# Kernel tuning notes

Measured on AMD Instinct MI355X. Metric: run time of the kernel, lower is better.

## Reference

```python
import jax, jax.numpy as jnp
import numpy as np

N_NODES = 50000
N_EDGES = 1600000
DIM_NODE = 64
DIM_HIDDEN = [64, 64]
EDGE_DIM = 32
NUM_CLASSES = 10
NUM_GRAPHS = 128


def _glorot(key, shape):
    fan_in, fan_out = shape[0], shape[1]
    lim = jnp.sqrt(6.0 / (fan_in + fan_out))
    return jax.random.uniform(key, shape, jnp.float32, -lim, lim)


def setup_inputs() -> dict:
    key = jax.random.key(0)
    ks = jax.random.split(key, 20)
    x = jax.random.normal(ks[0], (N_NODES, DIM_NODE), jnp.float32)
    edge_attr = jax.random.normal(ks[1], (N_EDGES, EDGE_DIM), jnp.float32)
    edge_index = jax.random.randint(ks[2], (2, N_EDGES), 0, N_NODES, jnp.int64)
    batch = jnp.sort(jax.random.randint(ks[3], (N_NODES,), 0, NUM_GRAPHS, jnp.int64))
    h0 = (DIM_NODE + DIM_HIDDEN[0]) // 2  # 64
    h1 = (DIM_HIDDEN[0] + DIM_HIDDEN[1]) // 2  # 64
    return {
        "x": x,
        "edge_attr": edge_attr,
        "We1": _glorot(ks[4], (EDGE_DIM, DIM_NODE)), "be1": jnp.zeros((DIM_NODE,), jnp.float32),
        "W1a": _glorot(ks[5], (DIM_NODE, h0)), "b1a": jnp.zeros((h0,), jnp.float32),
        "W1b": _glorot(ks[6], (h0, DIM_HIDDEN[0])), "b1b": jnp.zeros((DIM_HIDDEN[0],), jnp.float32),
        "We2": _glorot(ks[7], (EDGE_DIM, DIM_HIDDEN[0])), "be2": jnp.zeros((DIM_HIDDEN[0],), jnp.float32),
        "W2a": _glorot(ks[8], (DIM_HIDDEN[0], h1)), "b2a": jnp.zeros((h1,), jnp.float32),
        "W2b": _glorot(ks[9], (h1, DIM_HIDDEN[1])), "b2b": jnp.zeros((DIM_HIDDEN[1],), jnp.float32),
        "Wf": _glorot(ks[10], (DIM_HIDDEN[1], NUM_CLASSES)), "bf": jnp.zeros((NUM_CLASSES,), jnp.float32),
        "edge_index": edge_index,
        "batch": batch,
    }


def _gine_conv(x, edge_index, edge_attr, We, be, Wa, ba, Wb, bb):
    # PyG GINEConv (eps=0): msg = relu(x_src + lin_edge(edge_attr)),
    # aggr = scatter_sum(msg -> dst), out = nn(x + aggr)
    src, dst = edge_index[0], edge_index[1]
    e = edge_attr @ We + be                      # [E, d]
    m = jax.nn.relu(x[src] + e)                  # [E, d] gather + add + relu
    aggr = jax.ops.segment_sum(m, dst, num_segments=x.shape[0])  # [N, d]
    h = x + aggr
    h = h @ Wa + ba
    h = h @ Wb + bb
    return h


def reference(x, edge_attr, We1, be1, W1a, b1a, W1b, b1b,
              We2, be2, W2a, b2a, W2b, b2b, Wf, bf,
              edge_index, batch):
    h = jax.nn.relu(_gine_conv(x, edge_index, edge_attr, We1, be1, W1a, b1a, W1b, b1b))
    h = jax.nn.relu(_gine_conv(h, edge_index, edge_attr, We2, be2, W2a, b2a, W2b, b2b))
    # global mean pool per graph
    sums = jax.ops.segment_sum(h, batch, num_segments=NUM_GRAPHS)
    cnts = jax.ops.segment_sum(jnp.ones((h.shape[0],), h.dtype), batch, num_segments=NUM_GRAPHS)
    pooled = sums / jnp.clip(cnts, 1.0)[:, None]
    # ffn: (dropout p=0 in eval) -> linear -> softmax
    logits = pooled @ Wf + bf
    return jax.nn.softmax(logits, axis=1)
```

## Files before the change

kernel.cpp:

```cpp
#include <hip/hip_runtime.h>

#define N_NODES 50000
#define N_EDGES 1600000
#define DIM 64
#define EDIM 32
#define NUM_GRAPHS 128
#define NUM_CLASSES 10
#define NBIN_PAD 50176
#define NSCAN_BLK 196
#define EPAD_MAX 2200000
#define NBUCK 196
#define BCAP 12288
#define ACH 4096

typedef __attribute__((ext_vector_type(8))) short bf16x8;
typedef __attribute__((ext_vector_type(4))) short short4v;
typedef __attribute__((ext_vector_type(4))) unsigned short ushort4v;
typedef __attribute__((ext_vector_type(4))) float f32x4;

static __device__ __forceinline__ short f2bf(float f) {
    unsigned u = __builtin_bit_cast(unsigned, f);
    u += 0x7fff + ((u >> 16) & 1);
    return (short)(u >> 16);
}
static __device__ __forceinline__ float bf2f(short s) {
    unsigned u = ((unsigned)(unsigned short)s) << 16;
    return __builtin_bit_cast(float, u);
}
static __device__ __forceinline__ int cvt_pk_bf16(float lo, float hi) {
    int r;
    asm("v_cvt_pk_bf16_f32 %0, %1, %2" : "=v"(r) : "v"(lo), "v"(hi));
    return r;
}

__global__ void __launch_bounds__(256) binA_kernel(
    const int* __restrict__ src, const int* __restrict__ dst,
    int* __restrict__ bcur, int2* __restrict__ bbuf)
{
    __shared__ int hist[256];
    __shared__ int scanb[256];
    __shared__ int bexcl[256];
    __shared__ int cursA[256];
    __shared__ int gbase[256];
    __shared__ int2 st[ACH];

    const int t = threadIdx.x;
    const int e0 = blockIdx.x * ACH;
    const int nv = min(ACH, N_EDGES - e0);

    hist[t] = 0;
    __syncthreads();

    int w1[ACH / 256];
    #pragma unroll
    for (int i = 0; i < ACH / 256; ++i) {
        int idx = t + 256 * i;
        if (idx < nv) {
            int e = e0 + idx;
            int d = dst[e], s = src[e];
            w1[i] = (s & 0xFFFF) | (d << 16);
            atomicAdd(&hist[(unsigned)w1[i] >> 24], 1);
        } else {
            w1[i] = -1;
        }
    }
    __syncthreads();

    int v = hist[t];
    scanb[t] = v;
    __syncthreads();
    #pragma unroll
    for (int off = 1; off < 256; off <<= 1) {
        int add = (t >= off) ? scanb[t - off] : 0;
        __syncthreads();
        scanb[t] += add;
        __syncthreads();
    }
    int excl = scanb[t] - v;
    bexcl[t] = excl;
    cursA[t] = excl;
    if (v > 0) gbase[t] = atomicAdd(&bcur[t], v);
    __syncthreads();

    #pragma unroll
    for (int i = 0; i < ACH / 256; ++i) {
        int idx = t + 256 * i;
        if (idx < nv) {
            int b = (unsigned)w1[i] >> 24;
            int r = atomicAdd(&cursA[b], 1);
            int2 rec; rec.x = e0 + idx; rec.y = w1[i];
            st[r] = rec;
        }
    }
    __syncthreads();

    for (int k = t; k < nv; k += 256) {
        int2 rec = st[k];
        int b = (unsigned)rec.y >> 24;
        int pos = gbase[b] + (k - bexcl[b]);
        if (pos < BCAP) bbuf[(size_t)b * BCAP + pos] = rec;
    }
}

__global__ void __launch_bounds__(1024) binB1_kernel(
    const int* __restrict__ bcur, const int2* __restrict__ bbuf,
    int* __restrict__ cnt)
{
    __shared__ int nodecnt[256];
    const int b = blockIdx.x, t = threadIdx.x;
    if (t < 256) nodecnt[t] = 0;
    __syncthreads();
    const int nb = min(bcur[b], BCAP);
    for (int k = t; k < nb; k += 1024) {
        int2 rec = bbuf[(size_t)b * BCAP + k];
        int dlow = ((unsigned)rec.y >> 16) & 0xFF;
        atomicAdd(&nodecnt[dlow], 1);
    }
    __syncthreads();
    if (t < 256) cnt[b * 256 + t] = nodecnt[t];
}

__global__ void scan_part(const int* __restrict__ cnt, int* __restrict__ pstart,
                          int* __restrict__ partial) {
    __shared__ int sh[256];
    const int b = blockIdx.x, t = threadIdx.x;
    const int i = b * 256 + t;
    int v = ((cnt[i] + 15) >> 4) << 4;
    sh[t] = v;
    __syncthreads();
    #pragma unroll
    for (int off = 1; off < 256; off <<= 1) {
        int add = (t >= off) ? sh[t - off] : 0;
        __syncthreads();
        sh[t] += add;
        __syncthreads();
    }
    pstart[i] = sh[t] - v;
    if (t == 255) partial[b] = sh[t];
}

__global__ void scan_mid(int* __restrict__ partial) {
    __shared__ int sh[256];
    const int t = threadIdx.x;
    int v = (t < NSCAN_BLK) ? partial[t] : 0;
    sh[t] = v;
    __syncthreads();
    #pragma unroll
    for (int off = 1; off < 256; off <<= 1) {
        int add = (t >= off) ? sh[t - off] : 0;
        __syncthreads();
        sh[t] += add;
        __syncthreads();
    }
    if (t < NSCAN_BLK) partial[t] = sh[t] - v;
}

__global__ void scan_add(int* __restrict__ pstart, const int* __restrict__ partial) {
    const int b = blockIdx.x, t = threadIdx.x;
    const int i = b * 256 + t;
    pstart[i] += partial[b];
}

__global__ void __launch_bounds__(1024) binB2_kernel(
    const int* __restrict__ bcur, const int2* __restrict__ bbuf,
    const int* __restrict__ pstart, const int* __restrict__ cnt,
    const float* __restrict__ ea,
    unsigned short* __restrict__ ssrc, short* __restrict__ eab,
    int* __restrict__ tnode, float* __restrict__ aggr)
{
    __shared__ int cur[256];
    const int b = blockIdx.x, t = threadIdx.x;
    if (t < 256) cur[t] = pstart[b * 256 + t];
    __syncthreads();
    const int nb = min(bcur[b], BCAP);
    for (int k = t; k < nb; k += 1024) {
        int2 rec = bbuf[(size_t)b * BCAP + k];
        unsigned y = (unsigned)rec.y;
        int dlow = (y >> 16) & 0xFF;
        int p = atomicAdd(&cur[dlow], 1);
        ssrc[p] = (unsigned short)(y & 0xFFFF);
        const float* ar = ea + (size_t)rec.x * EDIM;
        int* er = (int*)(eab + (size_t)p * 32);
        #pragma unroll
        for (int qq = 0; qq < 4; ++qq) {
            float4 lo = *reinterpret_cast<const float4*>(ar + 4 * qq);
            float4 hi = *reinterpret_cast<const float4*>(ar + 4 * qq + 16);
            int4 w;
            w.x = cvt_pk_bf16(lo.x, lo.y);
            w.y = cvt_pk_bf16(lo.z, lo.w);
            w.z = cvt_pk_bf16(hi.x, hi.y);
            w.w = cvt_pk_bf16(hi.z, hi.w);
            *reinterpret_cast<int4*>(er + 4 * qq) = w;
        }
    }
    __syncthreads();
    if (t < 256) {
        int n = b * 256 + t;
        if (n < N_NODES) {
            int p0 = pstart[n], deg = cnt[n];
            int pe = p0 + (((deg + 15) >> 4) << 4);
            int4 z; z.x = 0; z.y = 0; z.z = 0; z.w = 0;
            for (int p = p0 + deg; p < pe; ++p) {
                ssrc[p] = (unsigned short)N_NODES;
                int4* er = (int4*)(eab + (size_t)p * 32);
                er[0] = z; er[1] = z; er[2] = z; er[3] = z;
            }
            for (int tt = p0 >> 4; tt < (pe >> 4); ++tt) tnode[tt] = n;
            if (deg == 0) {
                float4 z4; z4.x = 0.f; z4.y = 0.f; z4.z = 0.f; z4.w = 0.f;
                float4* arow = (float4*)(aggr + (size_t)n * 64);
                #pragma unroll
                for (int j = 0; j < 16; ++j) arow[j] = z4;
            }
        }
    }
}

__global__ void xprep_kernel(const float* __restrict__ x, short* __restrict__ xb,
                             short* __restrict__ hb) {
    int t = blockIdx.x * blockDim.x + threadIdx.x;
    if (t >= (N_NODES + 1) * 64) return;
    int n = t >> 6, k = t & 63;
    if (n == N_NODES) {
        short pz = f2bf(-1e30f);
        xb[t] = pz;
        hb[t] = pz;
        return;
    }
    int dim = 16 * (k & 3) + (k >> 2);
    xb[(size_t)n * 64 + k] = f2bf(x[(size_t)n * 64 + dim]);
}

__global__ void __launch_bounds__(256) edge_kernel(
    const short* __restrict__ xb,
    const short* __restrict__ eab,
    const unsigned short* __restrict__ ssrc,
    const float* __restrict__ We,
    const float* __restrict__ be,
    const int*   __restrict__ tnode,
    const int*   __restrict__ pstart,
    float* __restrict__ aggr)
{
    const int lane = threadIdx.x & 63;
    const int q = lane >> 4;
    const int c = lane & 15;
    const int wave  = (blockIdx.x * blockDim.x + threadIdx.x) >> 6;
    const int nwav  = (gridDim.x * blockDim.x) >> 6;

    const int ntiles = pstart[N_NODES] >> 4;
    int t0 = (int)(((long long)ntiles * wave) / nwav);
    int t1 = (int)(((long long)ntiles * (wave + 1)) / nwav);
    while (t0 > 0 && t0 < ntiles && tnode[t0] == tnode[t0 - 1]) ++t0;
    while (t1 > 0 && t1 < ntiles && tnode[t1] == tnode[t1 - 1]) ++t1;
    if (t0 >= t1) return;

    bf16x8 bfrag[4];
    #pragma unroll
    for (int t = 0; t < 4; ++t) {
        #pragma unroll
        for (int e = 0; e < 8; ++e) {
            int k = 4 * q + (e & 3) + 16 * (e >> 2);
            bfrag[t][e] = f2bf(We[k * 64 + 16 * t + c]);
        }
    }
    f32x4 cb[4];
    #pragma unroll
    for (int t = 0; t < 4; ++t) {
        float bv = be[16 * t + c];
        cb[t][0] = bv; cb[t][1] = bv; cb[t][2] = bv; cb[t][3] = bv;
    }

    auto clampT = [&](int tt) { return tt < t1 ? tt : t1 - 1; };
    auto loadIdx = [&](int tt, int& tn, ushort4v& s4) {
        tn = tnode[tt];
        s4 = *reinterpret_cast<const ushort4v*>(ssrc + tt * 16 + 4 * q);
    };
    auto loadE = [&](int tt) {
        return *reinterpret_cast<const bf16x8*>(eab + (size_t)tt * 512 + c * 32 + q * 8);
    };

    int prev_n = -1;
    float acc0 = 0.f, acc1 = 0.f, acc2 = 0.f, acc3 = 0.f;

    auto flush = [&](int n) {
        float r0 = acc0 + __shfl_xor(acc0, 16, 64);
        float r1 = acc1 + __shfl_xor(acc1, 16, 64);
        float r2 = acc2 + __shfl_xor(acc2, 16, 64);
        float r3 = acc3 + __shfl_xor(acc3, 16, 64);
        r0 += __shfl_xor(r0, 32, 64);
        r1 += __shfl_xor(r1, 32, 64);
        r2 += __shfl_xor(r2, 32, 64);
        r3 += __shfl_xor(r3, 32, 64);
        float v = (q == 0) ? r0 : (q == 1) ? r1 : (q == 2) ? r2 : r3;
        aggr[(size_t)n * 64 + lane] = v;
    };

    int tnA, tnB;
    ushort4v s4A, s4B;
    loadIdx(t0, tnA, s4A);
    loadIdx(clampT(t0 + 1), tnB, s4B);
    bf16x8 efA = loadE(t0);
    short4v xvA0 = *reinterpret_cast<const short4v*>(xb + (size_t)s4A.x * 64 + 4 * c);
    short4v xvA1 = *reinterpret_cast<const short4v*>(xb + (size_t)s4A.y * 64 + 4 * c);
    short4v xvA2 = *reinterpret_cast<const short4v*>(xb + (size_t)s4A.z * 64 + 4 * c);
    short4v xvA3 = *reinterpret_cast<const short4v*>(xb + (size_t)s4A.w * 64 + 4 * c);

    for (int tile = t0; tile < t1; ++tile) {
        bf16x8 efB = loadE(clampT(tile + 1));
        short4v yv0 = *reinterpret_cast<const short4v*>(xb + (size_t)s4B.x * 64 + 4 * c);
        short4v yv1 = *reinterpret_cast<const short4v*>(xb + (size_t)s4B.y * 64 + 4 * c);
        short4v yv2 = *reinterpret_cast<const short4v*>(xb + (size_t)s4B.z * 64 + 4 * c);
        short4v yv3 = *reinterpret_cast<const short4v*>(xb + (size_t)s4B.w * 64 + 4 * c);
        int tnC; ushort4v s4C;
        loadIdx(clampT(tile + 2), tnC, s4C);

        if (tnA != prev_n) {
            if (prev_n >= 0) flush(prev_n);
            prev_n = tnA;
            acc0 = acc1 = acc2 = acc3 = 0.f;
        }

        f32x4 d[4];
        #pragma unroll
        for (int t = 0; t < 4; ++t)
            d[t] = __builtin_amdgcn_mfma_f32_16x16x32_bf16(efA, bfrag[t], cb[t], 0, 0, 0);

        const short4v xv[4] = {xvA0, xvA1, xvA2, xvA3};
        #pragma unroll
        for (int r = 0; r < 4; ++r) {
            acc0 += fmaxf(d[0][r] + bf2f(xv[r][0]), 0.f);
            acc1 += fmaxf(d[1][r] + bf2f(xv[r][1]), 0.f);
            acc2 += fmaxf(d[2][r] + bf2f(xv[r][2]), 0.f);
            acc3 += fmaxf(d[3][r] + bf2f(xv[r][3]), 0.f);
        }

        tnA = tnB; s4A = s4B;
        tnB = tnC; s4B = s4C;
        efA = efB;
        xvA0 = yv0; xvA1 = yv1; xvA2 = yv2; xvA3 = yv3;
    }
    if (prev_n >= 0) flush(prev_n);
}

__global__ void __launch_bounds__(256) node_kernel(
    const float* __restrict__ x,
    const float* __restrict__ aggr,
    const float* __restrict__ Wab,
    const float* __restrict__ bab,
    float* __restrict__ out,
    short* __restrict__ hb)
{
    const int lane = threadIdx.x & 63;
    const int q = lane >> 4;
    const int c = lane & 15;
    const int wave = (blockIdx.x * blockDim.x + threadIdx.x) >> 6;
    const int nwav = (gridDim.x * blockDim.x) >> 6;

    bf16x8 bfrag[2][4];
    #pragma unroll
    for (int kk = 0; kk < 2; ++kk) {
        #pragma unroll
        for (int t = 0; t < 4; ++t) {
            #pragma unroll
            for (int e = 0; e < 8; ++e) {
                int k = 32 * kk + 4 * q + (e & 3) + 16 * (e >> 2);
                bfrag[kk][t][e] = f2bf(Wab[k * 64 + 16 * t + c]);
            }
        }
    }
    f32x4 cb[4];
    #pragma unroll
    for (int t = 0; t < 4; ++t) {
        float bv = bab[16 * t + c];
        cb[t][0] = bv; cb[t][1] = bv; cb[t][2] = bv; cb[t][3] = bv;
    }

    const int ntile = N_NODES / 16;
    for (int nt = wave; nt < ntile; nt += nwav) {
        const int n0 = nt * 16;
        const float* xr = x    + (size_t)(n0 + c) * 64;
        const float* ar = aggr + (size_t)(n0 + c) * 64;
        float4 v[4];
        #pragma unroll
        for (int j = 0; j < 4; ++j) {
            int off = (j >> 1) * 32 + (j & 1) * 16 + 4 * q;
            float4 a = *reinterpret_cast<const float4*>(xr + off);
            float4 b = *reinterpret_cast<const float4*>(ar + off);
            v[j].x = a.x + b.x; v[j].y = a.y + b.y;
            v[j].z = a.z + b.z; v[j].w = a.w + b.w;
        }
        f32x4 d[4];
        #pragma unroll
        for (int kk = 0; kk < 2; ++kk) {
            int4 ai;
            ai.x = cvt_pk_bf16(v[2 * kk].x, v[2 * kk].y);
            ai.y = cvt_pk_bf16(v[2 * kk].z, v[2 * kk].w);
            ai.z = cvt_pk_bf16(v[2 * kk + 1].x, v[2 * kk + 1].y);
            ai.w = cvt_pk_bf16(v[2 * kk + 1].z, v[2 * kk + 1].w);
            bf16x8 afrag = __builtin_bit_cast(bf16x8, ai);
            #pragma unroll
            for (int t = 0; t < 4; ++t)
                d[t] = __builtin_amdgcn_mfma_f32_16x16x32_bf16(
                    afrag, bfrag[kk][t], kk == 0 ? cb[t] : d[t], 0, 0, 0);
        }
        #pragma unroll
        for (int r = 0; r < 4; ++r) {
            float h0 = fmaxf(d[0][r], 0.f);
            float h1v = fmaxf(d[1][r], 0.f);
            float h2v = fmaxf(d[2][r], 0.f);
            float h3 = fmaxf(d[3][r], 0.f);
            float* orow = out + (size_t)(n0 + 4 * q + r) * 64;
            orow[c]      = h0;
            orow[16 + c] = h1v;
            orow[32 + c] = h2v;
            orow[48 + c] = h3;
            int2 pk;
            pk.x = cvt_pk_bf16(h0, h1v);
            pk.y = cvt_pk_bf16(h2v, h3);
            *reinterpret_cast<int2*>(hb + (size_t)(n0 + 4 * q + r) * 64 + 4 * c) = pk;
        }
    }
}

__global__ void prep_kernel(
    const float* __restrict__ Wa1, const float* __restrict__ ba1,
    const float* __restrict__ Wb1, const float* __restrict__ bb1,
    const float* __restrict__ Wa2, const float* __restrict__ ba2,
    const float* __restrict__ Wb2, const float* __restrict__ bb2,
    float* __restrict__ Wab1, float* __restrict__ bab1,
    float* __restrict__ Wab2, float* __restrict__ bab2)
{
    const int t = threadIdx.x;
    for (int idx = t; idx < 64 * 64; idx += 256) {
        int i = idx >> 6, j = idx & 63;
        float s1 = 0.f, s2 = 0.f;
        for (int m = 0; m < 64; ++m) {
            s1 += Wa1[i * 64 + m] * Wb1[m * 64 + j];
            s2 += Wa2[i * 64 + m] * Wb2[m * 64 + j];
        }
        Wab1[idx] = s1; Wab2[idx] = s2;
    }
    for (int j = t; j < 64; j += 256) {
        float s1 = bb1[j], s2 = bb2[j];
        for (int m = 0; m < 64; ++m) {
            s1 += ba1[m] * Wb1[m * 64 + j];
            s2 += ba2[m] * Wb2[m * 64 + j];
        }
        bab1[j] = s1; bab2[j] = s2;
    }
}

__global__ void __launch_bounds__(256) pool_kernel(
    const float* __restrict__ h,
    const int*   __restrict__ batch,
    float* __restrict__ psum,
    float* __restrict__ pcnt)
{
    const int lane = threadIdx.x & 63;
    const int wave = (blockIdx.x * blockDim.x + threadIdx.x) >> 6;
    const int n0 = wave * 64;
    if (n0 >= N_NODES) return;
    const int nend = min(n0 + 64, N_NODES);

    int cur = batch[n0];
    float acc = 0.f;
    int cnt = 0;
    for (int n = n0; n < nend; ++n) {
        int b = batch[n];
        if (b != cur) {
            atomicAdd(&psum[(size_t)cur * 64 + lane], acc);
            if (lane == 0) atomicAdd(&pcnt[cur], (float)cnt);
            cur = b; acc = 0.f; cnt = 0;
        }
        acc += h[(size_t)n * 64 + lane];
        cnt++;
    }
    atomicAdd(&psum[(size_t)cur * 64 + lane], acc);
    if (lane == 0) atomicAdd(&pcnt[cur], (float)cnt);
}

__global__ void final_kernel(
    const float* __restrict__ psum, const float* __restrict__ pcnt,
    const float* __restrict__ Wf, const float* __restrict__ bfv,
    float* __restrict__ out)
{
    __shared__ float pooled[NUM_GRAPHS * 64];
    __shared__ float logits[NUM_GRAPHS * NUM_CLASSES];
    const int t = threadIdx.x;
    for (int idx = t; idx < NUM_GRAPHS * 64; idx += 256) {
        int g = idx >> 6;
        float cc = pcnt[g];
        cc = cc < 1.f ? 1.f : cc;
        pooled[idx] = psum[idx] / cc;
    }
    __syncthreads();
    for (int idx = t; idx < NUM_GRAPHS * NUM_CLASSES; idx += 256) {
        int g = idx / NUM_CLASSES, cc = idx % NUM_CLASSES;
        float acc = bfv[cc];
        for (int k = 0; k < 64; ++k)
            acc += pooled[g * 64 + k] * Wf[k * NUM_CLASSES + cc];
        logits[idx] = acc;
    }
    __syncthreads();
    if (t < NUM_GRAPHS) {
        float mx = -1e30f;
        for (int cc = 0; cc < NUM_CLASSES; ++cc)
            mx = fmaxf(mx, logits[t * NUM_CLASSES + cc]);
        float s = 0.f;
        float ex[NUM_CLASSES];
        for (int cc = 0; cc < NUM_CLASSES; ++cc) {
            ex[cc] = expf(logits[t * NUM_CLASSES + cc] - mx);
            s += ex[cc];
        }
        for (int cc = 0; cc < NUM_CLASSES; ++cc)
            out[t * NUM_CLASSES + cc] = ex[cc] / s;
    }
}

extern "C" void kernel_launch(void* const* d_in, const int* in_sizes, int n_in,
                              void* d_out, int out_size, void* d_ws, size_t ws_size,
                              hipStream_t stream) {
    const float* x   = (const float*)d_in[0];
    const float* ea  = (const float*)d_in[1];
    const float* We1 = (const float*)d_in[2];
    const float* be1 = (const float*)d_in[3];
    const float* W1a = (const float*)d_in[4];
    const float* b1a = (const float*)d_in[5];
    const float* W1b = (const float*)d_in[6];
    const float* b1b = (const float*)d_in[7];
    const float* We2 = (const float*)d_in[8];
    const float* be2 = (const float*)d_in[9];
    const float* W2a = (const float*)d_in[10];
    const float* b2a = (const float*)d_in[11];
    const float* W2b = (const float*)d_in[12];
    const float* b2b = (const float*)d_in[13];
    const float* Wf  = (const float*)d_in[14];
    const float* bfv = (const float*)d_in[15];
    const int* ei    = (const int*)d_in[16];
    const int* batch = (const int*)d_in[17];
    const int* src = ei;
    const int* dst = ei + N_EDGES;

    int* wsb = (int*)d_ws;
    float* aggr = (float*)wsb;
    float* h1   = (float*)(wsb + 3200000);
    float* h2   = (float*)(wsb + 6400000);
    short* eab  = (short*)(wsb + 9600000);
    int2*  bbuf = (int2*)(wsb + 44800000);
    short* xb   = (short*)(wsb + 49616896);
    short* hb1  = (short*)(wsb + 51216928);
    short* hb2  = (short*)(wsb + 52816960);
    unsigned short* ssrc = (unsigned short*)(wsb + 54416992);
    int* tnode  = wsb + 55516992;
    float* Wab1 = (float*)(wsb + 55654492);
    float* bab1 = Wab1 + 4096;
    float* Wab2 = bab1 + 64;
    float* bab2 = Wab2 + 4096;
    float* psum = bab2 + 64;
    float* pcnt = psum + 8192;
    int* cnt    = (int*)(pcnt + 128);
    int* pstart = cnt + NBIN_PAD;
    int* partial= pstart + NBIN_PAD;
    int* bcur   = partial + 256;

    float* out = (float*)d_out;

    hipMemsetAsync(bcur, 0, 256 * sizeof(int), stream);
    binA_kernel<<<(N_EDGES + ACH - 1) / ACH, 256, 0, stream>>>(src, dst, bcur, bbuf);
    binB1_kernel<<<NBUCK, 1024, 0, stream>>>(bcur, bbuf, cnt);
    scan_part<<<NSCAN_BLK, 256, 0, stream>>>(cnt, pstart, partial);
    scan_mid<<<1, 256, 0, stream>>>(partial);
    scan_add<<<NSCAN_BLK, 256, 0, stream>>>(pstart, partial);
    binB2_kernel<<<NBUCK, 1024, 0, stream>>>(bcur, bbuf, pstart, cnt, ea,
                                             ssrc, eab, tnode, aggr);
    xprep_kernel<<<((N_NODES + 1) * 64 + 255) / 256, 256, 0, stream>>>(x, xb, hb1);

    hipMemsetAsync(psum, 0, (8192 + 128) * sizeof(float), stream);
    prep_kernel<<<1, 256, 0, stream>>>(W1a, b1a, W1b, b1b, W2a, b2a, W2b, b2b,
                                       Wab1, bab1, Wab2, bab2);

    edge_kernel<<<2048, 256, 0, stream>>>(xb, eab, ssrc, We1, be1, tnode, pstart, aggr);
    node_kernel<<<512, 256, 0, stream>>>(x, aggr, Wab1, bab1, h1, hb1);

    edge_kernel<<<2048, 256, 0, stream>>>(hb1, eab, ssrc, We2, be2, tnode, pstart, aggr);
    node_kernel<<<512, 256, 0, stream>>>(h1, aggr, Wab2, bab2, h2, hb2);

    pool_kernel<<<196, 256, 0, stream>>>(h2, batch, psum, pcnt);
    final_kernel<<<1, 256, 0, stream>>>(psum, pcnt, Wf, bfv, out);
}
```

Measured before the change: 396.6 us.

## Precompute per-edge ranks and split edge placement into many parallel blocks

binB1 now records each edge's rank within its destination node, so the placement pass no longer needs shared-memory atomics. That lets placement run across 8x more blocks (196*8 blocks of 256 threads), each handling a slice of a bucket, with two edges per thread to overlap the gathers of edge attributes. Padding and tnode setup move to a separate kernel. The cost is an extra rank array written and read, plus one more launch. The rank16 buffer is placed after bcur in the workspace, and it is not visible whether that region is large enough.

```diff
diff --git a/kernel.cpp b/kernel.cpp
--- a/kernel.cpp
+++ b/kernel.cpp
@@ -12,6 +12,7 @@
 #define NBUCK 196
 #define BCAP 12288
 #define ACH 4096
+#define NSL 8
 
 typedef __attribute__((ext_vector_type(8))) short bf16x8;
 typedef __attribute__((ext_vector_type(4))) short short4v;
@@ -104,7 +105,7 @@
 
 __global__ void __launch_bounds__(1024) binB1_kernel(
     const int* __restrict__ bcur, const int2* __restrict__ bbuf,
-    int* __restrict__ cnt)
+    int* __restrict__ cnt, unsigned short* __restrict__ rank16)
 {
     __shared__ int nodecnt[256];
     const int b = blockIdx.x, t = threadIdx.x;
@@ -112,9 +113,11 @@
     __syncthreads();
     const int nb = min(bcur[b], BCAP);
     for (int k = t; k < nb; k += 1024) {
-        int2 rec = bbuf[(size_t)b * BCAP + k];
+        size_t i = (size_t)b * BCAP + k;
+        int2 rec = bbuf[i];
         int dlow = ((unsigned)rec.y >> 16) & 0xFF;
-        atomicAdd(&nodecnt[dlow], 1);
+        int r = atomicAdd(&nodecnt[dlow], 1);
+        rank16[i] = (unsigned short)r;
     }
     __syncthreads();
     if (t < 256) cnt[b * 256 + t] = nodecnt[t];
@@ -161,58 +164,90 @@
     pstart[i] += partial[b];
 }
 
-__global__ void __launch_bounds__(1024) binB2_kernel(
+__global__ void __launch_bounds__(256) place_kernel(
     const int* __restrict__ bcur, const int2* __restrict__ bbuf,
+    const unsigned short* __restrict__ rank16,
+    const int* __restrict__ pstart, const float* __restrict__ ea,
+    unsigned short* __restrict__ ssrc, short* __restrict__ eab)
+{
+    const int b  = blockIdx.x >> 3;
+    const int sl = blockIdx.x & (NSL - 1);
+    const int t  = threadIdx.x;
+    const int nb = min(bcur[b], BCAP);
+    const int chunk = (nb + NSL - 1) / NSL;
+    const int k0 = sl * chunk;
+    const int k1 = min(k0 + chunk, nb);
+
+    for (int k = k0 + t; k < k1; k += 512) {
+        const int kb = k + 256;
+        const bool has2 = kb < k1;
+        const size_t i1 = (size_t)b * BCAP + k;
+        const size_t i2 = has2 ? (size_t)b * BCAP + kb : i1;
+        int2 rec1 = bbuf[i1];
+        int2 rec2 = bbuf[i2];
+        int rk1 = rank16[i1];
+        int rk2 = rank16[i2];
+        unsigned y1 = (unsigned)rec1.y, y2 = (unsigned)rec2.y;
+        int n1 = (b << 8) | ((y1 >> 16) & 0xFF);
+        int n2 = (b << 8) | ((y2 >> 16) & 0xFF);
+        int p1 = pstart[n1] + rk1;
+        int p2 = pstart[n2] + rk2;
+        const float* ar1 = ea + (size_t)rec1.x * EDIM;
+        const float* ar2 = ea + (size_t)rec2.x * EDIM;
+        float4 v1[8], v2[8];
+        #pragma unroll
+        for (int qq = 0; qq < 4; ++qq) {
+            v1[qq]     = *reinterpret_cast<const float4*>(ar1 + 4 * qq);
+            v1[qq + 4] = *reinterpret_cast<const float4*>(ar1 + 4 * qq + 16);
+            v2[qq]     = *reinterpret_cast<const float4*>(ar2 + 4 * qq);
+            v2[qq + 4] = *reinterpret_cast<const float4*>(ar2 + 4 * qq + 16);
+        }
+        ssrc[p1] = (unsigned short)(y1 & 0xFFFF);
+        ssrc[p2] = (unsigned short)(y2 & 0xFFFF);
+        int* er1 = (int*)(eab + (size_t)p1 * 32);
+        int* er2 = (int*)(eab + (size_t)p2 * 32);
+        #pragma unroll
+        for (int qq = 0; qq < 4; ++qq) {
+            int4 w;
+            w.x = cvt_pk_bf16(v1[qq].x, v1[qq].y);
+            w.y = cvt_pk_bf16(v1[qq].z, v1[qq].w);
+            w.z = cvt_pk_bf16(v1[qq + 4].x, v1[qq + 4].y);
+            w.w = cvt_pk_bf16(v1[qq + 4].z, v1[qq + 4].w);
+            *reinterpret_cast<int4*>(er1 + 4 * qq) = w;
+        }
+        #pragma unroll
+        for (int qq = 0; qq < 4; ++qq) {
+            int4 w;
+            w.x = cvt_pk_bf16(v2[qq].x, v2[qq].y);
+            w.y = cvt_pk_bf16(v2[qq].z, v2[qq].w);
+            w.z = cvt_pk_bf16(v2[qq + 4].x, v2[qq + 4].y);
+            w.w = cvt_pk_bf16(v2[qq + 4].z, v2[qq + 4].w);
+            *reinterpret_cast<int4*>(er2 + 4 * qq) = w;
+        }
+    }
+}
+
+__global__ void __launch_bounds__(256) pad_kernel(
     const int* __restrict__ pstart, const int* __restrict__ cnt,
-    const float* __restrict__ ea,
     unsigned short* __restrict__ ssrc, short* __restrict__ eab,
     int* __restrict__ tnode, float* __restrict__ aggr)
 {
-    __shared__ int cur[256];
-    const int b = blockIdx.x, t = threadIdx.x;
-    if (t < 256) cur[t] = pstart[b * 256 + t];
-    __syncthreads();
-    const int nb = min(bcur[b], BCAP);
-    for (int k = t; k < nb; k += 1024) {
-        int2 rec = bbuf[(size_t)b * BCAP + k];
-        unsigned y = (unsigned)rec.y;
-        int dlow = (y >> 16) & 0xFF;
-        int p = atomicAdd(&cur[dlow], 1);
-        ssrc[p] = (unsigned short)(y & 0xFFFF);
-        const float* ar = ea + (size_t)rec.x * EDIM;
-        int* er = (int*)(eab + (size_t)p * 32);
-        #pragma unroll
-        for (int qq = 0; qq < 4; ++qq) {
-            float4 lo = *reinterpret_cast<const float4*>(ar + 4 * qq);
-            float4 hi = *reinterpret_cast<const float4*>(ar + 4 * qq + 16);
-            int4 w;
-            w.x = cvt_pk_bf16(lo.x, lo.y);
-            w.y = cvt_pk_bf16(lo.z, lo.w);
-            w.z = cvt_pk_bf16(hi.x, hi.y);
-            w.w = cvt_pk_bf16(hi.z, hi.w);
-            *reinterpret_cast<int4*>(er + 4 * qq) = w;
-        }
-    }
-    __syncthreads();
-    if (t < 256) {
-        int n = b * 256 + t;
-        if (n < N_NODES) {
-            int p0 = pstart[n], deg = cnt[n];
-            int pe = p0 + (((deg + 15) >> 4) << 4);
-            int4 z; z.x = 0; z.y = 0; z.z = 0; z.w = 0;
-            for (int p = p0 + deg; p < pe; ++p) {
-                ssrc[p] = (unsigned short)N_NODES;
-                int4* er = (int4*)(eab + (size_t)p * 32);
-                er[0] = z; er[1] = z; er[2] = z; er[3] = z;
-            }
-            for (int tt = p0 >> 4; tt < (pe >> 4); ++tt) tnode[tt] = n;
-            if (deg == 0) {
-                float4 z4; z4.x = 0.f; z4.y = 0.f; z4.z = 0.f; z4.w = 0.f;
-                float4* arow = (float4*)(aggr + (size_t)n * 64);
-                #pragma unroll
-                for (int j = 0; j < 16; ++j) arow[j] = z4;
-            }
-        }
+    int n = blockIdx.x * 256 + threadIdx.x;
+    if (n >= N_NODES) return;
+    int p0 = pstart[n], deg = cnt[n];
+    int pe = p0 + (((deg + 15) >> 4) << 4);
+    int4 z; z.x = 0; z.y = 0; z.z = 0; z.w = 0;
+    for (int p = p0 + deg; p < pe; ++p) {
+        ssrc[p] = (unsigned short)N_NODES;
+        int4* er = (int4*)(eab + (size_t)p * 32);
+        er[0] = z; er[1] = z; er[2] = z; er[3] = z;
+    }
+    for (int tt = p0 >> 4; tt < (pe >> 4); ++tt) tnode[tt] = n;
+    if (deg == 0) {
+        float4 z4; z4.x = 0.f; z4.y = 0.f; z4.z = 0.f; z4.w = 0.f;
+        float4* arow = (float4*)(aggr + (size_t)n * 64);
+        #pragma unroll
+        for (int j = 0; j < 16; ++j) arow[j] = z4;
     }
 }
 
@@ -562,17 +597,19 @@
     int* pstart = cnt + NBIN_PAD;
     int* partial= pstart + NBIN_PAD;
     int* bcur   = partial + 256;
+    unsigned short* rank16 = (unsigned short*)(bcur + 256);
 
     float* out = (float*)d_out;
 
     hipMemsetAsync(bcur, 0, 256 * sizeof(int), stream);
     binA_kernel<<<(N_EDGES + ACH - 1) / ACH, 256, 0, stream>>>(src, dst, bcur, bbuf);
-    binB1_kernel<<<NBUCK, 1024, 0, stream>>>(bcur, bbuf, cnt);
+    binB1_kernel<<<NBUCK, 1024, 0, stream>>>(bcur, bbuf, cnt, rank16);
     scan_part<<<NSCAN_BLK, 256, 0, stream>>>(cnt, pstart, partial);
     scan_mid<<<1, 256, 0, stream>>>(partial);
     scan_add<<<NSCAN_BLK, 256, 0, stream>>>(pstart, partial);
-    binB2_kernel<<<NBUCK, 1024, 0, stream>>>(bcur, bbuf, pstart, cnt, ea,
-                                             ssrc, eab, tnode, aggr);
+    place_kernel<<<NBUCK * NSL, 256, 0, stream>>>(bcur, bbuf, rank16, pstart, ea,
+                                                  ssrc, eab);
+    pad_kernel<<<NSCAN_BLK, 256, 0, stream>>>(pstart, cnt, ssrc, eab, tnode, aggr);
     xprep_kernel<<<((N_NODES + 1) * 64 + 255) / 256, 256, 0, stream>>>(x, xb, hb1);
 
     hipMemsetAsync(psum, 0, (8192 + 128) * sizeof(float), stream);
```

Result: no change. 403.4 us (+1.7%).

## Split edge binning into rank, position, coalesced edge-attr scatter, and pad kernels

Applied to the files above, without the earlier changes.

binB1 now records each edge's intra-node rank, so final positions can be computed without a second atomic pass. A new pos_kernel writes per-edge destination positions and source ids. A separate grid-wide kernel then reads edge_attr in original order (coalesced) and scatters bf16 rows, replacing random gathers done by only 196 blocks. Padding work moves to its own kernel; this adds extra launches and a pos buffer in the workspace.

```diff
diff --git a/kernel.cpp b/kernel.cpp
--- a/kernel.cpp
+++ b/kernel.cpp
@@ -104,7 +104,7 @@
 
 __global__ void __launch_bounds__(1024) binB1_kernel(
     const int* __restrict__ bcur, const int2* __restrict__ bbuf,
-    int* __restrict__ cnt)
+    int* __restrict__ cnt, unsigned short* __restrict__ rank16)
 {
     __shared__ int nodecnt[256];
     const int b = blockIdx.x, t = threadIdx.x;
@@ -112,9 +112,11 @@
     __syncthreads();
     const int nb = min(bcur[b], BCAP);
     for (int k = t; k < nb; k += 1024) {
-        int2 rec = bbuf[(size_t)b * BCAP + k];
+        size_t i = (size_t)b * BCAP + k;
+        int2 rec = bbuf[i];
         int dlow = ((unsigned)rec.y >> 16) & 0xFF;
-        atomicAdd(&nodecnt[dlow], 1);
+        int r = atomicAdd(&nodecnt[dlow], 1);
+        rank16[i] = (unsigned short)r;
     }
     __syncthreads();
     if (t < 256) cnt[b * 256 + t] = nodecnt[t];
@@ -161,58 +163,68 @@
     pstart[i] += partial[b];
 }
 
-__global__ void __launch_bounds__(1024) binB2_kernel(
+__global__ void __launch_bounds__(1024) pos_kernel(
     const int* __restrict__ bcur, const int2* __restrict__ bbuf,
+    const unsigned short* __restrict__ rank16, const int* __restrict__ pstart,
+    int* __restrict__ pos, unsigned short* __restrict__ ssrc)
+{
+    const int b = blockIdx.x, t = threadIdx.x;
+    const int nb = min(bcur[b], BCAP);
+    for (int k = t; k < nb; k += 1024) {
+        size_t i = (size_t)b * BCAP + k;
+        int2 rec = bbuf[i];
+        unsigned y = (unsigned)rec.y;
+        int n = (b << 8) | ((y >> 16) & 0xFF);
+        int p = pstart[n] + (int)rank16[i];
+        pos[rec.x] = p;
+        ssrc[p] = (unsigned short)(y & 0xFFFF);
+    }
+}
+
+__global__ void __launch_bounds__(256) eascatter_kernel(
+    const float* __restrict__ ea, const int* __restrict__ pos,
+    short* __restrict__ eab)
+{
+    int e = blockIdx.x * 256 + threadIdx.x;
+    if (e >= N_EDGES) return;
+    int p = pos[e];
+    if ((unsigned)p >= (unsigned)EPAD_MAX) return;
+    const float* ar = ea + (size_t)e * EDIM;
+    int4 w[4];
+    #pragma unroll
+    for (int qq = 0; qq < 4; ++qq) {
+        float4 lo = *reinterpret_cast<const float4*>(ar + 4 * qq);
+        float4 hi = *reinterpret_cast<const float4*>(ar + 4 * qq + 16);
+        w[qq].x = cvt_pk_bf16(lo.x, lo.y);
+        w[qq].y = cvt_pk_bf16(lo.z, lo.w);
+        w[qq].z = cvt_pk_bf16(hi.x, hi.y);
+        w[qq].w = cvt_pk_bf16(hi.z, hi.w);
+    }
+    int4* er = (int4*)(eab + (size_t)p * 32);
+    er[0] = w[0]; er[1] = w[1]; er[2] = w[2]; er[3] = w[3];
+}
+
+__global__ void __launch_bounds__(256) pad_kernel(
     const int* __restrict__ pstart, const int* __restrict__ cnt,
-    const float* __restrict__ ea,
     unsigned short* __restrict__ ssrc, short* __restrict__ eab,
     int* __restrict__ tnode, float* __restrict__ aggr)
 {
-    __shared__ int cur[256];
-    const int b = blockIdx.x, t = threadIdx.x;
-    if (t < 256) cur[t] = pstart[b * 256 + t];
-    __syncthreads();
-    const int nb = min(bcur[b], BCAP);
-    for (int k = t; k < nb; k += 1024) {
-        int2 rec = bbuf[(size_t)b * BCAP + k];
-        unsigned y = (unsigned)rec.y;
-        int dlow = (y >> 16) & 0xFF;
-        int p = atomicAdd(&cur[dlow], 1);
-        ssrc[p] = (unsigned short)(y & 0xFFFF);
-        const float* ar = ea + (size_t)rec.x * EDIM;
-        int* er = (int*)(eab + (size_t)p * 32);
-        #pragma unroll
-        for (int qq = 0; qq < 4; ++qq) {
-            float4 lo = *reinterpret_cast<const float4*>(ar + 4 * qq);
-            float4 hi = *reinterpret_cast<const float4*>(ar + 4 * qq + 16);
-            int4 w;
-            w.x = cvt_pk_bf16(lo.x, lo.y);
-            w.y = cvt_pk_bf16(lo.z, lo.w);
-            w.z = cvt_pk_bf16(hi.x, hi.y);
-            w.w = cvt_pk_bf16(hi.z, hi.w);
-            *reinterpret_cast<int4*>(er + 4 * qq) = w;
-        }
-    }
-    __syncthreads();
-    if (t < 256) {
-        int n = b * 256 + t;
-        if (n < N_NODES) {
-            int p0 = pstart[n], deg = cnt[n];
-            int pe = p0 + (((deg + 15) >> 4) << 4);
-            int4 z; z.x = 0; z.y = 0; z.z = 0; z.w = 0;
-            for (int p = p0 + deg; p < pe; ++p) {
-                ssrc[p] = (unsigned short)N_NODES;
-                int4* er = (int4*)(eab + (size_t)p * 32);
-                er[0] = z; er[1] = z; er[2] = z; er[3] = z;
-            }
-            for (int tt = p0 >> 4; tt < (pe >> 4); ++tt) tnode[tt] = n;
-            if (deg == 0) {
-                float4 z4; z4.x = 0.f; z4.y = 0.f; z4.z = 0.f; z4.w = 0.f;
-                float4* arow = (float4*)(aggr + (size_t)n * 64);
-                #pragma unroll
-                for (int j = 0; j < 16; ++j) arow[j] = z4;
-            }
-        }
+    int n = blockIdx.x * 256 + threadIdx.x;
+    if (n >= N_NODES) return;
+    int p0 = pstart[n], deg = cnt[n];
+    int pe = p0 + (((deg + 15) >> 4) << 4);
+    int4 z; z.x = 0; z.y = 0; z.z = 0; z.w = 0;
+    for (int p = p0 + deg; p < pe; ++p) {
+        ssrc[p] = (unsigned short)N_NODES;
+        int4* er = (int4*)(eab + (size_t)p * 32);
+        er[0] = z; er[1] = z; er[2] = z; er[3] = z;
+    }
+    for (int tt = p0 >> 4; tt < (pe >> 4); ++tt) tnode[tt] = n;
+    if (deg == 0) {
+        float4 z4; z4.x = 0.f; z4.y = 0.f; z4.z = 0.f; z4.w = 0.f;
+        float4* arow = (float4*)(aggr + (size_t)n * 64);
+        #pragma unroll
+        for (int j = 0; j < 16; ++j) arow[j] = z4;
     }
 }
 
@@ -562,17 +574,20 @@
     int* pstart = cnt + NBIN_PAD;
     int* partial= pstart + NBIN_PAD;
     int* bcur   = partial + 256;
+    unsigned short* rank16 = (unsigned short*)(bcur + 256);
+    int* pos    = (int*)(rank16 + (size_t)NBUCK * BCAP);
 
     float* out = (float*)d_out;
 
     hipMemsetAsync(bcur, 0, 256 * sizeof(int), stream);
     binA_kernel<<<(N_EDGES + ACH - 1) / ACH, 256, 0, stream>>>(src, dst, bcur, bbuf);
-    binB1_kernel<<<NBUCK, 1024, 0, stream>>>(bcur, bbuf, cnt);
+    binB1_kernel<<<NBUCK, 1024, 0, stream>>>(bcur, bbuf, cnt, rank16);
     scan_part<<<NSCAN_BLK, 256, 0, stream>>>(cnt, pstart, partial);
     scan_mid<<<1, 256, 0, stream>>>(partial);
     scan_add<<<NSCAN_BLK, 256, 0, stream>>>(pstart, partial);
-    binB2_kernel<<<NBUCK, 1024, 0, stream>>>(bcur, bbuf, pstart, cnt, ea,
-                                             ssrc, eab, tnode, aggr);
+    pos_kernel<<<NBUCK, 1024, 0, stream>>>(bcur, bbuf, rank16, pstart, pos, ssrc);
+    eascatter_kernel<<<(N_EDGES + 255) / 256, 256, 0, stream>>>(ea, pos, eab);
+    pad_kernel<<<NSCAN_BLK, 256, 0, stream>>>(pstart, cnt, ssrc, eab, tnode, aggr);
     xprep_kernel<<<((N_NODES + 1) * 64 + 255) / 256, 256, 0, stream>>>(x, xb, hb1);
 
     hipMemsetAsync(psum, 0, (8192 + 128) * sizeof(float), stream);
```

Result: no change. 391.2 us (-1.4%).

## Convert edge attributes to bf16 during coarse binning and carry them through buckets

Applied to the files above, without the earlier changes.

Edge-attribute bf16 conversion moves out of the second binning pass and into the first, where each chunk reads edge_attr sequentially and stages the converted rows in shared memory before writing them per bucket. The second pass then copies 64-byte bf16 rows within a bucket instead of gathering fp32 rows at random edge ids. This trades a scattered 128-byte gather for an extra 64-byte write and read of a bucketed edge buffer, and makes the binning chunk smaller with a large shared-memory stage.

```diff
diff --git a/kernel.cpp b/kernel.cpp
--- a/kernel.cpp
+++ b/kernel.cpp
@@ -11,7 +11,7 @@
 #define EPAD_MAX 2200000
 #define NBUCK 196
 #define BCAP 12288
-#define ACH 4096
+#define ACH 1792
 
 typedef __attribute__((ext_vector_type(8))) short bf16x8;
 typedef __attribute__((ext_vector_type(4))) short short4v;
@@ -33,77 +33,99 @@
     return r;
 }
 
-__global__ void __launch_bounds__(256) binA_kernel(
+__global__ void __launch_bounds__(512) binAE_kernel(
     const int* __restrict__ src, const int* __restrict__ dst,
-    int* __restrict__ bcur, int2* __restrict__ bbuf)
+    const float* __restrict__ ea,
+    int* __restrict__ bcur, short* __restrict__ bbufE, int* __restrict__ bbufR)
 {
     __shared__ int hist[256];
     __shared__ int scanb[256];
     __shared__ int bexcl[256];
     __shared__ int cursA[256];
     __shared__ int gbase[256];
-    __shared__ int2 st[ACH];
+    __shared__ int stR[ACH];
+    __shared__ short stE[ACH * 32];
 
     const int t = threadIdx.x;
     const int e0 = blockIdx.x * ACH;
     const int nv = min(ACH, N_EDGES - e0);
 
-    hist[t] = 0;
-    __syncthreads();
-
-    int w1[ACH / 256];
-    #pragma unroll
-    for (int i = 0; i < ACH / 256; ++i) {
-        int idx = t + 256 * i;
+    if (t < 256) hist[t] = 0;
+    __syncthreads();
+
+    int w1[4];
+    #pragma unroll
+    for (int i = 0; i < 4; ++i) {
+        int idx = t + 512 * i;
+        w1[i] = -1;
         if (idx < nv) {
             int e = e0 + idx;
-            int d = dst[e], s = src[e];
-            w1[i] = (s & 0xFFFF) | (d << 16);
+            w1[i] = (src[e] & 0xFFFF) | (dst[e] << 16);
             atomicAdd(&hist[(unsigned)w1[i] >> 24], 1);
-        } else {
-            w1[i] = -1;
-        }
-    }
-    __syncthreads();
-
-    int v = hist[t];
-    scanb[t] = v;
-    __syncthreads();
-    #pragma unroll
+        }
+    }
+    __syncthreads();
+
+    int v = (t < 256) ? hist[t] : 0;
+    if (t < 256) scanb[t] = v;
+    __syncthreads();
     for (int off = 1; off < 256; off <<= 1) {
-        int add = (t >= off) ? scanb[t - off] : 0;
+        int add = (t >= off && t < 256) ? scanb[t - off] : 0;
         __syncthreads();
-        scanb[t] += add;
+        if (t < 256) scanb[t] += add;
         __syncthreads();
     }
-    int excl = scanb[t] - v;
-    bexcl[t] = excl;
-    cursA[t] = excl;
-    if (v > 0) gbase[t] = atomicAdd(&bcur[t], v);
-    __syncthreads();
-
-    #pragma unroll
-    for (int i = 0; i < ACH / 256; ++i) {
-        int idx = t + 256 * i;
+    if (t < 256) {
+        int excl = scanb[t] - v;
+        bexcl[t] = excl;
+        cursA[t] = excl;
+        if (v > 0) gbase[t] = atomicAdd(&bcur[t], v);
+    }
+    __syncthreads();
+
+    #pragma unroll
+    for (int i = 0; i < 4; ++i) {
+        int idx = t + 512 * i;
         if (idx < nv) {
             int b = (unsigned)w1[i] >> 24;
             int r = atomicAdd(&cursA[b], 1);
-            int2 rec; rec.x = e0 + idx; rec.y = w1[i];
-            st[r] = rec;
-        }
-    }
-    __syncthreads();
-
-    for (int k = t; k < nv; k += 256) {
-        int2 rec = st[k];
-        int b = (unsigned)rec.y >> 24;
-        int pos = gbase[b] + (k - bexcl[b]);
-        if (pos < BCAP) bbuf[(size_t)b * BCAP + pos] = rec;
+            stR[r] = w1[i];
+            const float* ar = ea + (size_t)(e0 + idx) * EDIM;
+            int* er = (int*)(stE + r * 32);
+            #pragma unroll
+            for (int qq = 0; qq < 4; ++qq) {
+                float4 lo = *reinterpret_cast<const float4*>(ar + 4 * qq);
+                float4 hi = *reinterpret_cast<const float4*>(ar + 4 * qq + 16);
+                int4 w;
+                w.x = cvt_pk_bf16(lo.x, lo.y);
+                w.y = cvt_pk_bf16(lo.z, lo.w);
+                w.z = cvt_pk_bf16(hi.x, hi.y);
+                w.w = cvt_pk_bf16(hi.z, hi.w);
+                *reinterpret_cast<int4*>(er + 4 * qq) = w;
+            }
+        }
+    }
+    __syncthreads();
+
+    const int s = t & 3;
+    for (int base = 0; base < nv; base += 128) {
+        int k = base + (t >> 2);
+        if (k < nv) {
+            int w = stR[k];
+            int b = (unsigned)w >> 24;
+            int pos = gbase[b] + (k - bexcl[b]);
+            if (pos < BCAP) {
+                size_t ro = (size_t)b * BCAP + pos;
+                if (s == 0) bbufR[ro] = w;
+                *reinterpret_cast<int4*>(bbufE + ro * 32 + 8 * s) =
+                    *reinterpret_cast<const int4*>(stE + (size_t)k * 32 + 8 * s);
+            }
+        }
     }
 }
 
 __global__ void __launch_bounds__(1024) binB1_kernel(
-    const int* __restrict__ bcur, const int2* __restrict__ bbuf,
+    const int* __restrict__ bcur, const int* __restrict__ bbufR,
     int* __restrict__ cnt)
 {
     __shared__ int nodecnt[256];
@@ -112,9 +134,8 @@
     __syncthreads();
     const int nb = min(bcur[b], BCAP);
     for (int k = t; k < nb; k += 1024) {
-        int2 rec = bbuf[(size_t)b * BCAP + k];
-        int dlow = ((unsigned)rec.y >> 16) & 0xFF;
-        atomicAdd(&nodecnt[dlow], 1);
+        int w = bbufR[(size_t)b * BCAP + k];
+        atomicAdd(&nodecnt[((unsigned)w >> 16) & 0xFF], 1);
     }
     __syncthreads();
     if (t < 256) cnt[b * 256 + t] = nodecnt[t];
@@ -161,10 +182,10 @@
     pstart[i] += partial[b];
 }
 
-__global__ void __launch_bounds__(1024) binB2_kernel(
-    const int* __restrict__ bcur, const int2* __restrict__ bbuf,
-    const int* __restrict__ pstart, const int* __restrict__ cnt,
-    const float* __restrict__ ea,
+__global__ void __launch_bounds__(1024) placeB_kernel(
+    const int* __restrict__ bcur, const short* __restrict__ bbufE,
+    const int* __restrict__ bbufR, const int* __restrict__ pstart,
+    const int* __restrict__ cnt,
     unsigned short* __restrict__ ssrc, short* __restrict__ eab,
     int* __restrict__ tnode, float* __restrict__ aggr)
 {
@@ -174,24 +195,14 @@
     __syncthreads();
     const int nb = min(bcur[b], BCAP);
     for (int k = t; k < nb; k += 1024) {
-        int2 rec = bbuf[(size_t)b * BCAP + k];
-        unsigned y = (unsigned)rec.y;
-        int dlow = (y >> 16) & 0xFF;
+        size_t ro = (size_t)b * BCAP + k;
+        int w = bbufR[ro];
+        int dlow = ((unsigned)w >> 16) & 0xFF;
         int p = atomicAdd(&cur[dlow], 1);
-        ssrc[p] = (unsigned short)(y & 0xFFFF);
-        const float* ar = ea + (size_t)rec.x * EDIM;
-        int* er = (int*)(eab + (size_t)p * 32);
-        #pragma unroll
-        for (int qq = 0; qq < 4; ++qq) {
-            float4 lo = *reinterpret_cast<const float4*>(ar + 4 * qq);
-            float4 hi = *reinterpret_cast<const float4*>(ar + 4 * qq + 16);
-            int4 w;
-            w.x = cvt_pk_bf16(lo.x, lo.y);
-            w.y = cvt_pk_bf16(lo.z, lo.w);
-            w.z = cvt_pk_bf16(hi.x, hi.y);
-            w.w = cvt_pk_bf16(hi.z, hi.w);
-            *reinterpret_cast<int4*>(er + 4 * qq) = w;
-        }
+        ssrc[p] = (unsigned short)(w & 0xFFFF);
+        const int4* er = reinterpret_cast<const int4*>(bbufE + ro * 32);
+        int4* eo = reinterpret_cast<int4*>(eab + (size_t)p * 32);
+        eo[0] = er[0]; eo[1] = er[1]; eo[2] = er[2]; eo[3] = er[3];
     }
     __syncthreads();
     if (t < 256) {
@@ -202,8 +213,8 @@
             int4 z; z.x = 0; z.y = 0; z.z = 0; z.w = 0;
             for (int p = p0 + deg; p < pe; ++p) {
                 ssrc[p] = (unsigned short)N_NODES;
-                int4* er = (int4*)(eab + (size_t)p * 32);
-                er[0] = z; er[1] = z; er[2] = z; er[3] = z;
+                int4* eo = reinterpret_cast<int4*>(eab + (size_t)p * 32);
+                eo[0] = z; eo[1] = z; eo[2] = z; eo[3] = z;
             }
             for (int tt = p0 >> 4; tt < (pe >> 4); ++tt) tnode[tt] = n;
             if (deg == 0) {
@@ -546,13 +557,14 @@
     float* h1   = (float*)(wsb + 3200000);
     float* h2   = (float*)(wsb + 6400000);
     short* eab  = (short*)(wsb + 9600000);
-    int2*  bbuf = (int2*)(wsb + 44800000);
-    short* xb   = (short*)(wsb + 49616896);
-    short* hb1  = (short*)(wsb + 51216928);
-    short* hb2  = (short*)(wsb + 52816960);
-    unsigned short* ssrc = (unsigned short*)(wsb + 54416992);
-    int* tnode  = wsb + 55516992;
-    float* Wab1 = (float*)(wsb + 55654492);
+    short* bbufE= (short*)(wsb + 44800000);
+    int* bbufR  = wsb + 83335168;
+    short* xb   = (short*)(wsb + 85743616);
+    short* hb1  = (short*)(wsb + 87343648);
+    short* hb2  = (short*)(wsb + 88943680);
+    unsigned short* ssrc = (unsigned short*)(wsb + 90543712);
+    int* tnode  = wsb + 91643712;
+    float* Wab1 = (float*)(wsb + 91781212);
     float* bab1 = Wab1 + 4096;
     float* Wab2 = bab1 + 64;
     float* bab2 = Wab2 + 4096;
@@ -566,13 +578,14 @@
     float* out = (float*)d_out;
 
     hipMemsetAsync(bcur, 0, 256 * sizeof(int), stream);
-    binA_kernel<<<(N_EDGES + ACH - 1) / ACH, 256, 0, stream>>>(src, dst, bcur, bbuf);
-    binB1_kernel<<<NBUCK, 1024, 0, stream>>>(bcur, bbuf, cnt);
+    binAE_kernel<<<(N_EDGES + ACH - 1) / ACH, 512, 0, stream>>>(
+        src, dst, ea, bcur, bbufE, bbufR);
+    binB1_kernel<<<NBUCK, 1024, 0, stream>>>(bcur, bbufR, cnt);
     scan_part<<<NSCAN_BLK, 256, 0, stream>>>(cnt, pstart, partial);
     scan_mid<<<1, 256, 0, stream>>>(partial);
     scan_add<<<NSCAN_BLK, 256, 0, stream>>>(pstart, partial);
-    binB2_kernel<<<NBUCK, 1024, 0, stream>>>(bcur, bbuf, pstart, cnt, ea,
-                                             ssrc, eab, tnode, aggr);
+    placeB_kernel<<<NBUCK, 1024, 0, stream>>>(bcur, bbufE, bbufR, pstart, cnt,
+                                              ssrc, eab, tnode, aggr);
     xprep_kernel<<<((N_NODES + 1) * 64 + 255) / 256, 256, 0, stream>>>(x, xb, hb1);
 
     hipMemsetAsync(psum, 0, (8192 + 128) * sizeof(float), stream);
```

After: 423.1 us. 6.7% more time.
